# Performance work log

Measured on AMD Instinct MI355X. Metric: run time of the kernel, lower is better.

## Reference

```python
import jax, jax.numpy as jnp
import numpy as np

DIM = 128
EXPAND = 2
INTERNAL = DIM * EXPAND  # 256
MAX_SEQ = 2048
BATCH = 32
GATE_DECAY = 3.0


def _gated_cell(x, Wa, ba, Wi, bi, g):
    # x: [B,S,D]; Wa,Wi: [E,D]; ba,bi,g: [E]
    pa = jnp.einsum('bsd,ed->bse', x, Wa) + ba          # projected activation
    pi = jnp.einsum('bsd,ed->bse', x, Wi) + bi          # projected input
    reset_gate = jax.nn.sigmoid(pa)
    input_gate = jax.nn.sigmoid(pi)
    alpha = jax.nn.sigmoid(g)                           # [E]
    a = alpha / jnp.power(GATE_DECAY, reset_gate)       # adaptive alpha [B,S,E]
    u = jnp.sqrt(1.0 - a * a) * (input_gate * pi)       # per-step input [B,S,E]

    def step(h, au):
        a_t, u_t = au
        h = a_t * h + u_t
        return h, h

    h0 = jnp.zeros((x.shape[0], Wa.shape[0]), x.dtype)
    _, ys = jax.lax.scan(step, h0, (a.transpose(1, 0, 2), u.transpose(1, 0, 2)))
    return ys.transpose(1, 0, 2)                        # [B,S,E]


def _recency_weights(seq_len, dtype):
    w = jnp.exp(jnp.linspace(0.0, 3.0, MAX_SEQ))[:seq_len]
    return w.astype(dtype).reshape(1, -1, 1)


def setup_inputs() -> dict:
    key = jax.random.key(0)
    ks = jax.random.split(key, 12)
    std = 1.0 / np.sqrt(DIM)  # kaiming fan_in linear
    lo = float(np.log(0.9 / 0.1))
    hi = float(np.log(0.999 / 0.001))
    d = {
        'x': jax.random.normal(ks[0], (BATCH, MAX_SEQ, DIM), jnp.float32),
        'Wa_u': jax.random.normal(ks[1], (INTERNAL, DIM), jnp.float32) * std,
        'ba_u': jnp.zeros((INTERNAL,), jnp.float32),
        'Wi_u': jax.random.normal(ks[2], (INTERNAL, DIM), jnp.float32) * std,
        'bi_u': jnp.zeros((INTERNAL,), jnp.float32),
        'g_u': jax.random.uniform(ks[3], (INTERNAL,), jnp.float32, lo, hi),
        'Wa_w': jax.random.normal(ks[4], (INTERNAL, DIM), jnp.float32) * std,
        'ba_w': jnp.zeros((INTERNAL,), jnp.float32),
        'Wi_w': jax.random.normal(ks[5], (INTERNAL, DIM), jnp.float32) * std,
        'bi_w': jnp.zeros((INTERNAL,), jnp.float32),
        'g_w': jax.random.uniform(ks[6], (INTERNAL,), jnp.float32, lo, hi),
        'Wf': jax.random.normal(ks[7], (DIM, 4 * DIM), jnp.float32) * (1.0 / np.sqrt(4 * DIM)),
        'bf': jnp.zeros((DIM,), jnp.float32),
    }
    return d


def reference(x, Wa_u, ba_u, Wi_u, bi_u, g_u, Wa_w, ba_w, Wi_w, bi_w, g_w, Wf, bf):
    unweighted = _gated_cell(x, Wa_u, ba_u, Wi_u, bi_u, g_u)          # [B,S,2D]
    xw = x * _recency_weights(x.shape[1], x.dtype)
    weighted = _gated_cell(xw, Wa_w, ba_w, Wi_w, bi_w, g_w)           # [B,S,2D]
    combined = jnp.concatenate([unweighted, weighted], axis=-1)       # [B,S,4D]
    return jnp.einsum('bsf,df->bsd', combined, Wf) + bf               # [B,S,D]
```

## Files before the change

kernel.cpp:

```cpp
#include <hip/hip_runtime.h>
#include <hip/hip_fp16.h>
#include <cstddef>
#include <cstdint>

#define DIM 128
#define SEQ 2048
#define NB 32
#define NCH 512
#define NROWS (NB * SEQ)

typedef _Float16 half8 __attribute__((ext_vector_type(8)));
typedef float    f32x4 __attribute__((ext_vector_type(4)));

#define CMB_BYTES ((size_t)NROWS * NCH * 2)
#define WFG_OFF   CMB_BYTES
#define WFG_BYTES ((size_t)NCH * DIM * 2)
#define WS_NEEDED (WFG_OFF + WFG_BYTES)

__device__ __forceinline__ float sigf(float v) {
    return 1.0f / (1.0f + __expf(-v));
}

__global__ void k0_wfg(const float* __restrict__ Wf, _Float16* __restrict__ Wfg) {
    int o = blockIdx.x * 256 + threadIdx.x;
    int j    = o & 7;
    int lane = (o >> 3) & 63;
    int q    = lane >> 4, n16 = lane & 15;
    int ct   = (o >> 9) & 7;
    int ks   = (o >> 12) & 1;
    int kb   = o >> 13;
    int k = kb * 64 + ks * 32 + q * 8 + j;
    int n = ct * 16 + n16;
    Wfg[o] = (_Float16)Wf[n * NCH + k];
}

__global__ __launch_bounds__(256, 2) void kfused(
        const float* __restrict__ x,
        const float* __restrict__ Wa_u, const float* __restrict__ ba_u,
        const float* __restrict__ Wi_u, const float* __restrict__ bi_u,
        const float* __restrict__ g_u,
        const float* __restrict__ Wa_w, const float* __restrict__ ba_w,
        const float* __restrict__ Wi_w, const float* __restrict__ bi_w,
        const float* __restrict__ g_w,
        _Float16* __restrict__ cmb) {
    __shared__ _Float16 xs[64][136];
    __shared__ float2   seg[16][33];
    __shared__ float    pref[16][33];
    __shared__ float    carry[32];
    __shared__ _Float16 hbuf[64][40];

    const int tid  = threadIdx.x;
    const int lane = tid & 63;
    const int w    = tid >> 6;
    const int quad = lane >> 4;
    const int n16  = lane & 15;

    const int b  = blockIdx.x;
    const int cg = blockIdx.y;
    const int p  = cg >> 3;
    const int ebase = (cg & 7) * 32;

    const float* Wa  = p ? Wa_w : Wa_u;
    const float* Wi  = p ? Wi_w : Wi_u;
    const float* bap = p ? ba_w : ba_u;
    const float* bip = p ? bi_w : bi_u;
    const float* gp  = p ? g_w  : g_u;

    half8 bf[4][4];
#pragma unroll
    for (int ks = 0; ks < 4; ++ks)
#pragma unroll
        for (int nt = 0; nt < 4; ++nt) {
            int e = ebase + (nt & 1) * 16 + n16;
            const float* Wp = (nt >> 1) ? Wi : Wa;
            const float* src = Wp + (size_t)e * DIM + ks * 32 + quad * 8;
            float4 v0 = *(const float4*)src;
            float4 v1 = *(const float4*)(src + 4);
            half8 hv;
            hv[0] = (_Float16)v0.x; hv[1] = (_Float16)v0.y;
            hv[2] = (_Float16)v0.z; hv[3] = (_Float16)v0.w;
            hv[4] = (_Float16)v1.x; hv[5] = (_Float16)v1.y;
            hv[6] = (_Float16)v1.z; hv[7] = (_Float16)v1.w;
            bf[ks][nt] = hv;
        }

    float rba[2], rbi[2], ral[2];
#pragma unroll
    for (int hh = 0; hh < 2; ++hh) {
        int e = ebase + hh * 16 + n16;
        rba[hh] = bap[e];
        rbi[hh] = bip[e];
        ral[hh] = sigf(gp[e]);
    }

    if (tid < 32) carry[tid] = 0.0f;

    const float* xrow = x + (size_t)b * SEQ * DIM;
    _Float16* cmbb = cmb + (size_t)b * SEQ * NCH + cg * 32;

    __syncthreads();

    for (int t = 0; t < 32; ++t) {
        const int s0 = t * 64;

#pragma unroll
        for (int i = 0; i < 4; ++i) {
            int g = tid + i * 256;
            int r = g >> 4, d8 = g & 15;
            const float* srcx = xrow + (size_t)(s0 + r) * DIM + d8 * 8;
            float4 v0 = *(const float4*)srcx;
            float4 v1 = *(const float4*)(srcx + 4);
            half8 hv;
            hv[0] = (_Float16)v0.x; hv[1] = (_Float16)v0.y;
            hv[2] = (_Float16)v0.z; hv[3] = (_Float16)v0.w;
            hv[4] = (_Float16)v1.x; hv[5] = (_Float16)v1.y;
            hv[6] = (_Float16)v1.z; hv[7] = (_Float16)v1.w;
            *(half8*)&xs[r][d8 * 8] = hv;
        }
        __syncthreads();

        f32x4 acc[4];
#pragma unroll
        for (int nt = 0; nt < 4; ++nt) acc[nt] = (f32x4){0.f, 0.f, 0.f, 0.f};
#pragma unroll
        for (int ks = 0; ks < 4; ++ks) {
            half8 af = *(const half8*)&xs[w * 16 + n16][ks * 32 + quad * 8];
#pragma unroll
            for (int nt = 0; nt < 4; ++nt)
                acc[nt] = __builtin_amdgcn_mfma_f32_16x16x32_f16(af, bf[ks][nt], acc[nt], 0, 0, 0);
        }

        const int sbase = s0 + w * 16 + quad * 4;
        float a_s[2][4], u_s[2][4];
#pragma unroll
        for (int hh = 0; hh < 2; ++hh) {
            float A4 = 1.0f, U4 = 0.0f;
#pragma unroll
            for (int reg = 0; reg < 4; ++reg) {
                float sc = p ? __expf((float)(sbase + reg) * (3.0f / 2047.0f)) : 1.0f;
                float pa = fmaf(acc[hh][reg],     sc, rba[hh]);
                float pi = fmaf(acc[2 + hh][reg], sc, rbi[hh]);
                float rst = sigf(pa);
                float ig  = sigf(pi);
                float a   = ral[hh] * exp2f(-rst * 1.5849625007211562f);
                float u   = sqrtf(fmaxf(1.0f - a * a, 0.0f)) * ig * pi;
                a_s[hh][reg] = a; u_s[hh][reg] = u;
                A4 *= a;
                U4 = fmaf(a, U4, u);
            }
            seg[w * 4 + quad][hh * 16 + n16] = make_float2(A4, U4);
        }
        __syncthreads();

        if (tid < 32) {
            float H = carry[tid];
#pragma unroll
            for (int ts = 0; ts < 16; ++ts) {
                float2 AU = seg[ts][tid];
                pref[ts][tid] = H;
                H = fmaf(AU.x, H, AU.y);
            }
            carry[tid] = H;
        }
        __syncthreads();

#pragma unroll
        for (int hh = 0; hh < 2; ++hh) {
            float h = pref[w * 4 + quad][hh * 16 + n16];
#pragma unroll
            for (int reg = 0; reg < 4; ++reg) {
                h = fmaf(a_s[hh][reg], h, u_s[hh][reg]);
                hbuf[w * 16 + quad * 4 + reg][hh * 16 + n16] = (_Float16)h;
            }
        }
        __syncthreads();

        {
            int row = tid >> 2, part = tid & 3;
            half8 hv = *(const half8*)&hbuf[row][part * 8];
            *(half8*)(cmbb + (size_t)(s0 + row) * NCH + part * 8) = hv;
        }
    }
}

__global__ __launch_bounds__(256, 2) void k3_mfma(
        const _Float16* __restrict__ cmb, const _Float16* __restrict__ Wfg,
        const float* __restrict__ bfv, float* __restrict__ out) {
    __shared__ _Float16 As[16 * 512];
    __shared__ _Float16 Bs[16 * 512];

    const int tid  = threadIdx.x;
    const int lane = tid & 63;
    const int w    = tid >> 6;
    const int row0 = blockIdx.x * 128;
    const int q    = lane >> 4;
    const int nn   = lane & 15;

    f32x4 acc[2][8];
#pragma unroll
    for (int rt = 0; rt < 2; ++rt)
#pragma unroll
        for (int ct = 0; ct < 8; ++ct)
            acc[rt][ct] = (f32x4){0.0f, 0.0f, 0.0f, 0.0f};

    for (int kb = 0; kb < 8; ++kb) {
        const int kc = kb * 64;
#pragma unroll
        for (int i = 0; i < 4; ++i) {
            int f = tid + i * 256;
            int r = f >> 3, k8 = f & 7;
            uint4 v = *(const uint4*)(cmb + (size_t)(row0 + r) * NCH + kc + k8 * 8);
            int rt = r >> 4, m = r & 15, ks = k8 >> 2, qq = k8 & 3;
            *(uint4*)&As[(((rt * 2 + ks) * 64) + qq * 16 + m) * 8] = v;
        }
#pragma unroll
        for (int i = 0; i < 4; ++i) {
            int f = tid + i * 256;
            uint4 v = *(const uint4*)(Wfg + (size_t)kb * 8192 + (size_t)f * 8);
            *(uint4*)&Bs[(size_t)f * 8] = v;
        }
        __syncthreads();

#pragma unroll
        for (int ks = 0; ks < 2; ++ks) {
            half8 a0 = *(const half8*)&As[(((w * 2 + 0) * 2 + ks) * 512) + lane * 8];
            half8 a1 = *(const half8*)&As[(((w * 2 + 1) * 2 + ks) * 512) + lane * 8];
#pragma unroll
            for (int ct = 0; ct < 8; ++ct) {
                half8 bb = *(const half8*)&Bs[((ks * 8 + ct) * 512) + lane * 8];
                acc[0][ct] = __builtin_amdgcn_mfma_f32_16x16x32_f16(a0, bb, acc[0][ct], 0, 0, 0);
                acc[1][ct] = __builtin_amdgcn_mfma_f32_16x16x32_f16(a1, bb, acc[1][ct], 0, 0, 0);
            }
        }
        __syncthreads();
    }

#pragma unroll
    for (int rt = 0; rt < 2; ++rt) {
        int rbase = row0 + w * 32 + rt * 16 + q * 4;
#pragma unroll
        for (int ct = 0; ct < 8; ++ct) {
            int col = ct * 16 + nn;
            float bias = bfv[col];
#pragma unroll
            for (int reg = 0; reg < 4; ++reg)
                out[(size_t)(rbase + reg) * DIM + col] = acc[rt][ct][reg] + bias;
        }
    }
}

extern "C" void kernel_launch(void* const* d_in, const int* in_sizes, int n_in,
                              void* d_out, int out_size, void* d_ws, size_t ws_size,
                              hipStream_t stream) {
    if (ws_size < WS_NEEDED) return;

    const float* x    = (const float*)d_in[0];
    const float* Wa_u = (const float*)d_in[1];
    const float* ba_u = (const float*)d_in[2];
    const float* Wi_u = (const float*)d_in[3];
    const float* bi_u = (const float*)d_in[4];
    const float* g_u  = (const float*)d_in[5];
    const float* Wa_w = (const float*)d_in[6];
    const float* ba_w = (const float*)d_in[7];
    const float* Wi_w = (const float*)d_in[8];
    const float* bi_w = (const float*)d_in[9];
    const float* g_w  = (const float*)d_in[10];
    const float* Wf   = (const float*)d_in[11];
    const float* bfv  = (const float*)d_in[12];
    float* out = (float*)d_out;

    char* ws = (char*)d_ws;
    _Float16* cmb = (_Float16*)ws;
    _Float16* Wfg = (_Float16*)(ws + WFG_OFF);

    hipLaunchKernelGGL(k0_wfg, dim3(256), dim3(256), 0, stream, Wf, Wfg);
    hipLaunchKernelGGL(kfused, dim3(32, 16), dim3(256), 0, stream,
                       x, Wa_u, ba_u, Wi_u, bi_u, g_u,
                       Wa_w, ba_w, Wi_w, bi_w, g_w, cmb);
    hipLaunchKernelGGL(k3_mfma, dim3(512), dim3(256), 0, stream,
                       cmb, Wfg, bfv, out);
}
```

Before: 219.2 us.

## Pre-convert x to fp16, load A fragments directly, and register-prefetch the output GEMM

A prep kernel now converts x to fp16 once, writing it to the workspace, and also builds the Wf layout. The recurrence kernel reads fp16 x fragments straight from global memory with a one-tile prefetch instead of staging through LDS, keeps the projection weights in LDS rather than registers, and replaces the per-step exp for recency weights with a multiplicative recurrence. The output GEMM switches to smaller K-steps with register double-buffered global loads, and both kernels raise launch bounds to 4 waves per SIMD. Together these aim to cut x reread traffic across 16 column groups and to raise occupancy and latency hiding. The cost is an extra kernel pass over x and more LDS reads of weights.

```diff
diff --git a/kernel.cpp b/kernel.cpp
--- a/kernel.cpp
+++ b/kernel.cpp
@@ -15,27 +15,48 @@
 #define CMB_BYTES ((size_t)NROWS * NCH * 2)
 #define WFG_OFF   CMB_BYTES
 #define WFG_BYTES ((size_t)NCH * DIM * 2)
-#define WS_NEEDED (WFG_OFF + WFG_BYTES)
+#define XH_OFF    (WFG_OFF + WFG_BYTES)
+#define XH_BYTES  ((size_t)NROWS * DIM * 2)
+#define WS_NEEDED (XH_OFF + XH_BYTES)
 
 __device__ __forceinline__ float sigf(float v) {
     return 1.0f / (1.0f + __expf(-v));
 }
 
-__global__ void k0_wfg(const float* __restrict__ Wf, _Float16* __restrict__ Wfg) {
-    int o = blockIdx.x * 256 + threadIdx.x;
-    int j    = o & 7;
-    int lane = (o >> 3) & 63;
-    int q    = lane >> 4, n16 = lane & 15;
-    int ct   = (o >> 9) & 7;
-    int ks   = (o >> 12) & 1;
-    int kb   = o >> 13;
-    int k = kb * 64 + ks * 32 + q * 8 + j;
-    int n = ct * 16 + n16;
-    Wfg[o] = (_Float16)Wf[n * NCH + k];
-}
-
-__global__ __launch_bounds__(256, 2) void kfused(
-        const float* __restrict__ x,
+__global__ void k0_prep(const float* __restrict__ x, const float* __restrict__ Wf,
+                        _Float16* __restrict__ xh, _Float16* __restrict__ Wfg) {
+    int bid = blockIdx.x;
+    if (bid < 4096) {
+        int g = bid * 256 + threadIdx.x;
+        const float* src = x + (size_t)g * 8;
+        float4 v0 = *(const float4*)src;
+        float4 v1 = *(const float4*)(src + 4);
+        half8 hv;
+        hv[0] = (_Float16)v0.x; hv[1] = (_Float16)v0.y;
+        hv[2] = (_Float16)v0.z; hv[3] = (_Float16)v0.w;
+        hv[4] = (_Float16)v1.x; hv[5] = (_Float16)v1.y;
+        hv[6] = (_Float16)v1.z; hv[7] = (_Float16)v1.w;
+        *(half8*)(xh + (size_t)g * 8) = hv;
+    } else {
+        int t = (bid - 4096) * 256 + threadIdx.x;
+#pragma unroll
+        for (int i = 0; i < 8; ++i) {
+            int o = t * 8 + i;
+            int j    = o & 7;
+            int lane = (o >> 3) & 63;
+            int q    = lane >> 4, n16 = lane & 15;
+            int ct   = (o >> 9) & 7;
+            int ks   = (o >> 12) & 1;
+            int kb   = o >> 13;
+            int k = kb * 64 + ks * 32 + q * 8 + j;
+            int n = ct * 16 + n16;
+            Wfg[o] = (_Float16)Wf[n * NCH + k];
+        }
+    }
+}
+
+__global__ __launch_bounds__(256, 4) void kfused(
+        const _Float16* __restrict__ xh,
         const float* __restrict__ Wa_u, const float* __restrict__ ba_u,
         const float* __restrict__ Wi_u, const float* __restrict__ bi_u,
         const float* __restrict__ g_u,
@@ -43,7 +64,7 @@
         const float* __restrict__ Wi_w, const float* __restrict__ bi_w,
         const float* __restrict__ g_w,
         _Float16* __restrict__ cmb) {
-    __shared__ _Float16 xs[64][136];
+    __shared__ _Float16 Bs[8192];
     __shared__ float2   seg[16][33];
     __shared__ float    pref[16][33];
     __shared__ float    carry[32];
@@ -66,23 +87,23 @@
     const float* bip = p ? bi_w : bi_u;
     const float* gp  = p ? g_w  : g_u;
 
-    half8 bf[4][4];
-#pragma unroll
-    for (int ks = 0; ks < 4; ++ks)
-#pragma unroll
-        for (int nt = 0; nt < 4; ++nt) {
-            int e = ebase + (nt & 1) * 16 + n16;
-            const float* Wp = (nt >> 1) ? Wi : Wa;
-            const float* src = Wp + (size_t)e * DIM + ks * 32 + quad * 8;
-            float4 v0 = *(const float4*)src;
-            float4 v1 = *(const float4*)(src + 4);
-            half8 hv;
-            hv[0] = (_Float16)v0.x; hv[1] = (_Float16)v0.y;
-            hv[2] = (_Float16)v0.z; hv[3] = (_Float16)v0.w;
-            hv[4] = (_Float16)v1.x; hv[5] = (_Float16)v1.y;
-            hv[6] = (_Float16)v1.z; hv[7] = (_Float16)v1.w;
-            bf[ks][nt] = hv;
-        }
+    for (int sl = tid; sl < 1024; sl += 256) {
+        int l  = sl & 63;
+        int nt = (sl >> 6) & 3;
+        int ks = sl >> 8;
+        int qq = l >> 4, nn = l & 15;
+        int e = ebase + (nt & 1) * 16 + nn;
+        const float* Wp = (nt >> 1) ? Wi : Wa;
+        const float* src = Wp + (size_t)e * DIM + ks * 32 + qq * 8;
+        float4 v0 = *(const float4*)src;
+        float4 v1 = *(const float4*)(src + 4);
+        half8 hv;
+        hv[0] = (_Float16)v0.x; hv[1] = (_Float16)v0.y;
+        hv[2] = (_Float16)v0.z; hv[3] = (_Float16)v0.w;
+        hv[4] = (_Float16)v1.x; hv[5] = (_Float16)v1.y;
+        hv[6] = (_Float16)v1.z; hv[7] = (_Float16)v1.w;
+        *(half8*)&Bs[sl * 8] = hv;
+    }
 
     float rba[2], rbi[2], ral[2];
 #pragma unroll
@@ -92,54 +113,62 @@
         rbi[hh] = bip[e];
         ral[hh] = sigf(gp[e]);
     }
-
     if (tid < 32) carry[tid] = 0.0f;
 
-    const float* xrow = x + (size_t)b * SEQ * DIM;
+    float scb = __expf((float)(w * 16 + quad * 4) * (3.0f / 2047.0f));
+    const float r1   = __expf(3.0f / 2047.0f);
+    const float r2   = r1 * r1;
+    const float r3   = r2 * r1;
+    const float cs64 = __expf(64.0f * 3.0f / 2047.0f);
+
+    const _Float16* xrow = xh + (size_t)b * SEQ * DIM;
     _Float16* cmbb = cmb + (size_t)b * SEQ * NCH + cg * 32;
 
     __syncthreads();
+
+    half8 af[4];
+    {
+        const _Float16* ab = xrow + (size_t)(w * 16 + n16) * DIM + quad * 8;
+#pragma unroll
+        for (int ks = 0; ks < 4; ++ks) af[ks] = *(const half8*)(ab + ks * 32);
+    }
 
     for (int t = 0; t < 32; ++t) {
         const int s0 = t * 64;
 
-#pragma unroll
-        for (int i = 0; i < 4; ++i) {
-            int g = tid + i * 256;
-            int r = g >> 4, d8 = g & 15;
-            const float* srcx = xrow + (size_t)(s0 + r) * DIM + d8 * 8;
-            float4 v0 = *(const float4*)srcx;
-            float4 v1 = *(const float4*)(srcx + 4);
-            half8 hv;
-            hv[0] = (_Float16)v0.x; hv[1] = (_Float16)v0.y;
-            hv[2] = (_Float16)v0.z; hv[3] = (_Float16)v0.w;
-            hv[4] = (_Float16)v1.x; hv[5] = (_Float16)v1.y;
-            hv[6] = (_Float16)v1.z; hv[7] = (_Float16)v1.w;
-            *(half8*)&xs[r][d8 * 8] = hv;
-        }
-        __syncthreads();
-
         f32x4 acc[4];
 #pragma unroll
         for (int nt = 0; nt < 4; ++nt) acc[nt] = (f32x4){0.f, 0.f, 0.f, 0.f};
 #pragma unroll
         for (int ks = 0; ks < 4; ++ks) {
-            half8 af = *(const half8*)&xs[w * 16 + n16][ks * 32 + quad * 8];
-#pragma unroll
-            for (int nt = 0; nt < 4; ++nt)
-                acc[nt] = __builtin_amdgcn_mfma_f32_16x16x32_f16(af, bf[ks][nt], acc[nt], 0, 0, 0);
-        }
-
-        const int sbase = s0 + w * 16 + quad * 4;
+            half8 a = af[ks];
+#pragma unroll
+            for (int nt = 0; nt < 4; ++nt) {
+                half8 bb = *(const half8*)&Bs[(ks * 256 + nt * 64 + lane) * 8];
+                acc[nt] = __builtin_amdgcn_mfma_f32_16x16x32_f16(a, bb, acc[nt], 0, 0, 0);
+            }
+        }
+
+        {
+            int tn = (t + 1) & 31;
+            const _Float16* ab = xrow + (size_t)(tn * 64 + w * 16 + n16) * DIM + quad * 8;
+#pragma unroll
+            for (int ks = 0; ks < 4; ++ks) af[ks] = *(const half8*)(ab + ks * 32);
+        }
+
+        float sc[4];
+        if (p) { sc[0] = scb; sc[1] = scb * r1; sc[2] = scb * r2; sc[3] = scb * r3; }
+        else   { sc[0] = sc[1] = sc[2] = sc[3] = 1.0f; }
+        scb *= cs64;
+
         float a_s[2][4], u_s[2][4];
 #pragma unroll
         for (int hh = 0; hh < 2; ++hh) {
             float A4 = 1.0f, U4 = 0.0f;
 #pragma unroll
             for (int reg = 0; reg < 4; ++reg) {
-                float sc = p ? __expf((float)(sbase + reg) * (3.0f / 2047.0f)) : 1.0f;
-                float pa = fmaf(acc[hh][reg],     sc, rba[hh]);
-                float pi = fmaf(acc[2 + hh][reg], sc, rbi[hh]);
+                float pa = fmaf(acc[hh][reg],     sc[reg], rba[hh]);
+                float pi = fmaf(acc[2 + hh][reg], sc[reg], rbi[hh]);
                 float rst = sigf(pa);
                 float ig  = sigf(pi);
                 float a   = ral[hh] * exp2f(-rst * 1.5849625007211562f);
@@ -183,11 +212,11 @@
     }
 }
 
-__global__ __launch_bounds__(256, 2) void k3_mfma(
+__global__ __launch_bounds__(256, 4) void k3_mfma(
         const _Float16* __restrict__ cmb, const _Float16* __restrict__ Wfg,
         const float* __restrict__ bfv, float* __restrict__ out) {
-    __shared__ _Float16 As[16 * 512];
-    __shared__ _Float16 Bs[16 * 512];
+    __shared__ _Float16 As[4096];
+    __shared__ _Float16 Bs[4096];
 
     const int tid  = threadIdx.x;
     const int lane = tid & 63;
@@ -203,34 +232,45 @@
         for (int ct = 0; ct < 8; ++ct)
             acc[rt][ct] = (f32x4){0.0f, 0.0f, 0.0f, 0.0f};
 
-    for (int kb = 0; kb < 8; ++kb) {
-        const int kc = kb * 64;
-#pragma unroll
-        for (int i = 0; i < 4; ++i) {
-            int f = tid + i * 256;
-            int r = f >> 3, k8 = f & 7;
-            uint4 v = *(const uint4*)(cmb + (size_t)(row0 + r) * NCH + kc + k8 * 8);
-            int rt = r >> 4, m = r & 15, ks = k8 >> 2, qq = k8 & 3;
-            *(uint4*)&As[(((rt * 2 + ks) * 64) + qq * 16 + m) * 8] = v;
-        }
-#pragma unroll
-        for (int i = 0; i < 4; ++i) {
-            int f = tid + i * 256;
-            uint4 v = *(const uint4*)(Wfg + (size_t)kb * 8192 + (size_t)f * 8);
-            *(uint4*)&Bs[(size_t)f * 8] = v;
-        }
-        __syncthreads();
-
-#pragma unroll
-        for (int ks = 0; ks < 2; ++ks) {
-            half8 a0 = *(const half8*)&As[(((w * 2 + 0) * 2 + ks) * 512) + lane * 8];
-            half8 a1 = *(const half8*)&As[(((w * 2 + 1) * 2 + ks) * 512) + lane * 8];
-#pragma unroll
-            for (int ct = 0; ct < 8; ++ct) {
-                half8 bb = *(const half8*)&Bs[((ks * 8 + ct) * 512) + lane * 8];
-                acc[0][ct] = __builtin_amdgcn_mfma_f32_16x16x32_f16(a0, bb, acc[0][ct], 0, 0, 0);
-                acc[1][ct] = __builtin_amdgcn_mfma_f32_16x16x32_f16(a1, bb, acc[1][ct], 0, 0, 0);
-            }
+    int fa[2], ra[2], k8a[2];
+#pragma unroll
+    for (int i = 0; i < 2; ++i) {
+        fa[i]  = tid + i * 256;
+        ra[i]  = fa[i] >> 2;
+        k8a[i] = fa[i] & 3;
+    }
+
+    uint4 pa[2], pb[2];
+#pragma unroll
+    for (int i = 0; i < 2; ++i) {
+        pa[i] = *(const uint4*)(cmb + (size_t)(row0 + ra[i]) * NCH + k8a[i] * 8);
+        pb[i] = *(const uint4*)(Wfg + (size_t)fa[i] * 8);
+    }
+
+    for (int kb2 = 0; kb2 < 16; ++kb2) {
+#pragma unroll
+        for (int i = 0; i < 2; ++i) {
+            *(uint4*)&As[(((ra[i] >> 4) * 64) + k8a[i] * 16 + (ra[i] & 15)) * 8] = pa[i];
+            *(uint4*)&Bs[(size_t)fa[i] * 8] = pb[i];
+        }
+        __syncthreads();
+
+        if (kb2 < 15) {
+            int kc = (kb2 + 1) * 32;
+#pragma unroll
+            for (int i = 0; i < 2; ++i) {
+                pa[i] = *(const uint4*)(cmb + (size_t)(row0 + ra[i]) * NCH + kc + k8a[i] * 8);
+                pb[i] = *(const uint4*)(Wfg + (size_t)(kb2 + 1) * 4096 + (size_t)fa[i] * 8);
+            }
+        }
+
+        half8 a0 = *(const half8*)&As[((w * 2 + 0) * 64 + lane) * 8];
+        half8 a1 = *(const half8*)&As[((w * 2 + 1) * 64 + lane) * 8];
+#pragma unroll
+        for (int ct = 0; ct < 8; ++ct) {
+            half8 bb = *(const half8*)&Bs[(ct * 64 + lane) * 8];
+            acc[0][ct] = __builtin_amdgcn_mfma_f32_16x16x32_f16(a0, bb, acc[0][ct], 0, 0, 0);
+            acc[1][ct] = __builtin_amdgcn_mfma_f32_16x16x32_f16(a1, bb, acc[1][ct], 0, 0, 0);
         }
         __syncthreads();
     }
@@ -272,10 +312,11 @@
     char* ws = (char*)d_ws;
     _Float16* cmb = (_Float16*)ws;
     _Float16* Wfg = (_Float16*)(ws + WFG_OFF);
-
-    hipLaunchKernelGGL(k0_wfg, dim3(256), dim3(256), 0, stream, Wf, Wfg);
+    _Float16* xh  = (_Float16*)(ws + XH_OFF);
+
+    hipLaunchKernelGGL(k0_prep, dim3(4128), dim3(256), 0, stream, x, Wf, xh, Wfg);
     hipLaunchKernelGGL(kfused, dim3(32, 16), dim3(256), 0, stream,
-                       x, Wa_u, ba_u, Wi_u, bi_u, g_u,
+                       xh, Wa_u, ba_u, Wi_u, bi_u, g_u,
                        Wa_w, ba_w, Wi_w, bi_w, g_w, cmb);
     hipLaunchKernelGGL(k3_mfma, dim3(512), dim3(256), 0, stream,
                        cmb, Wfg, bfv, out);
```

Result: slower. 241.0 us (+9.9%).
